# Kernel optimization log

Measured on AMD Instinct MI355X. Metric: run time of the kernel, lower is better.

## Reference

```python
import jax, jax.numpy as jnp
import numpy as np


def _swiglu(h):
    a, b = jnp.split(h, 2, axis=-1)
    return jax.nn.silu(a) * b


def setup_inputs() -> dict:
    key = jax.random.key(0)
    ks = jax.random.split(key, 12)
    B, T, D = 4, 2048, 1024
    HD = 4096          # dense FFN hidden (swiglu -> fc1 out 2*HD)
    S, K = 1024, 4     # ssm d_state, d_conv
    E, HE = 8, 512     # n_experts, expert hidden (swiglu)
    s = 0.02
    w = lambda k_, shape: jax.random.normal(k_, shape, jnp.float32) * s
    return dict(
        x=jax.random.normal(ks[0], (B, T, D), jnp.float32),
        rW=w(ks[1], (3, D)), rb=jnp.zeros((3,), jnp.float32),
        d1W=w(ks[2], (2 * HD, D)), d1b=jnp.zeros((2 * HD,), jnp.float32),
        d2W=w(ks[3], (D, HD)), d2b=jnp.zeros((D,), jnp.float32),
        sW_in=w(ks[4], (S, D)), sb_in=jnp.zeros((S,), jnp.float32),
        sW_conv=w(ks[5], (S, S, K)), sb_conv=jnp.zeros((S,), jnp.float32),
        sW_out=w(ks[6], (D, S)), sb_out=jnp.zeros((D,), jnp.float32),
        mW=w(ks[7], (E, D)), mb=jnp.zeros((E,), jnp.float32),
        eW1=w(ks[8], (E, 2 * HE, D)), eb1=jnp.zeros((E, 2 * HE), jnp.float32),
        eW2=w(ks[9], (E, D, HE)), eb2=jnp.zeros((E, D), jnp.float32),
        k=2,
    )


def reference(x, rW, rb, d1W, d1b, d2W, d2b,
              sW_in, sb_in, sW_conv, sb_conv, sW_out, sb_out,
              mW, mb, eW1, eb1, eW2, eb2, k):
    # ---- branch router (token-level softmax, temperature=1) ----
    bw = jax.nn.softmax(x @ rW.T + rb, axis=-1)              # [B,T,3]

    # ---- branch 0: dense swiglu FFN ----
    dense = _swiglu(x @ d1W.T + d1b) @ d2W.T + d2b           # [B,T,D]

    # ---- branch 1: SSM layer (causal conv, groups=1, gate=1) ----
    h = (x @ sW_in.T + sb_in).transpose(0, 2, 1)             # [B,S,T]
    Kc = sW_conv.shape[-1]
    conv = jax.lax.conv_general_dilated(
        h, sW_conv, window_strides=(1,), padding=[(Kc - 1, 0)],
        dimension_numbers=('NCH', 'OIH', 'NCH'))
    seq = (conv + sb_conv[None, :, None]).transpose(0, 2, 1)  # [B,T,S]
    ssm = seq @ sW_out.T + sb_out                             # [B,T,D]

    # ---- branch 2: MoE (top-k softmax router, dense-dispatch reference) ----
    E = mW.shape[0]
    logits = x @ mW.T + mb                                    # [B,T,E]
    vals, idx = jax.lax.top_k(logits, k)                      # [B,T,k]
    wk = jax.nn.softmax(vals, axis=-1)
    combine = jnp.sum(jax.nn.one_hot(idx, E, dtype=x.dtype) * wk[..., None], axis=-2)  # [B,T,E]
    h1 = _swiglu(jnp.einsum('btd,efd->btef', x, eW1) + eb1)   # [B,T,E,HE]
    eout = jnp.einsum('bteh,edh->bted', h1, eW2) + eb2        # [B,T,E,D]
    moe = jnp.einsum('bted,bte->btd', eout, combine)          # [B,T,D]

    return bw[..., 0:1] * dense + bw[..., 1:2] * ssm + bw[..., 2:3] * moe
```

## Files before the change

### kernel.cpp

```cpp
#include <hip/hip_runtime.h>
#include <hip/hip_bf16.h>
#include <cstdint>

typedef __bf16 bf16_t;
typedef __bf16 bf16x8 __attribute__((ext_vector_type(8)));
typedef float f32x4 __attribute__((ext_vector_type(4)));

#define DEV_INLINE __device__ __forceinline__

#define NTOK 8192
#define DDIM 1024
#define HDIM 4096
#define SDIM 1024
#define NEXP 8
#define HEXP 512
#define TSEQ 2048
#define MAXTILES 136
#define MAXROWS (MAXTILES * 128)

#define VMCNT(n) asm volatile("s_waitcnt vmcnt(" #n ")" ::: "memory")
#define BARF() asm volatile("s_barrier" ::: "memory")

__global__ __launch_bounds__(256) void k_f32_to_bf16(const float* __restrict__ src,
                                                     bf16_t* __restrict__ dst, int n8) {
  int i = blockIdx.x * 256 + threadIdx.x;
  if (i >= n8) return;
  const float4* s = (const float4*)src + (size_t)i * 2;
  float4 v0 = s[0], v1 = s[1];
  bf16x8 o;
  o[0] = (bf16_t)v0.x; o[1] = (bf16_t)v0.y; o[2] = (bf16_t)v0.z; o[3] = (bf16_t)v0.w;
  o[4] = (bf16_t)v1.x; o[5] = (bf16_t)v1.y; o[6] = (bf16_t)v1.z; o[7] = (bf16_t)v1.w;
  *((bf16x8*)dst + i) = o;
}

__global__ __launch_bounds__(256) void k_convw(const float* __restrict__ src,
                                               bf16_t* __restrict__ dst) {
  int i = blockIdx.x * 256 + threadIdx.x;
  size_t flat = (size_t)i * 8;
  int s = (int)(flat >> 12);
  int col = (int)(flat & 4095);
  int k = col >> 10;
  int si0 = col & 1023;
  const float* sp = src + (size_t)s * 4096 + k;
  bf16x8 o;
#pragma unroll
  for (int j = 0; j < 8; ++j) o[j] = (bf16_t)sp[(size_t)(si0 + j) * 4];
  *(bf16x8*)(dst + flat) = o;
}

__global__ __launch_bounds__(256) void k_im2col(const bf16_t* __restrict__ h,
                                                bf16_t* __restrict__ a2) {
  int i = blockIdx.x * 256 + threadIdx.x;
  size_t flat = (size_t)i * 8;
  int t = (int)(flat >> 12);
  int col = (int)(flat & 4095);
  int k = col >> 10;
  int si = col & 1023;
  int tt = t & (TSEQ - 1);
  bf16x8 v;
#pragma unroll
  for (int j = 0; j < 8; ++j) v[j] = (bf16_t)0.f;
  if (tt - 3 + k >= 0) v = *(const bf16x8*)(h + (size_t)(t - 3 + k) * SDIM + si);
  *(bf16x8*)(a2 + flat) = v;
}

__global__ __launch_bounds__(256) void k_zero(int* cnt, int* fill, int* idx,
                                              float* gate) {
  int i = blockIdx.x * 256 + threadIdx.x;
  if (i < NEXP) { cnt[i] = 0; fill[i] = 0; }
  if (i < MAXROWS) { idx[i] = 0; gate[i] = 0.f; }
}

__global__ __launch_bounds__(1024) void k_count(const int* __restrict__ top2e,
                                                int* __restrict__ cnt) {
  __shared__ int hist[NEXP];
  const int tid = threadIdx.x;
  if (tid < NEXP) hist[tid] = 0;
  __syncthreads();
  int c[NEXP];
#pragma unroll
  for (int e = 0; e < NEXP; ++e) c[e] = 0;
#pragma unroll
  for (int j = 0; j < 2 * NTOK / 1024; ++j) {
    int v = top2e[j * 1024 + tid];
#pragma unroll
    for (int e = 0; e < NEXP; ++e) c[e] += (v == e) ? 1 : 0;
  }
#pragma unroll
  for (int e = 0; e < NEXP; ++e)
    for (int off = 32; off; off >>= 1) c[e] += __shfl_xor(c[e], off);
  if ((tid & 63) == 0) {
#pragma unroll
    for (int e = 0; e < NEXP; ++e) atomicAdd(&hist[e], c[e]);
  }
  __syncthreads();
  if (tid < NEXP) cnt[tid] = hist[tid];
}

__global__ void k_scan(const int* __restrict__ cnt, int* __restrict__ base,
                       int* __restrict__ ntiles, int* __restrict__ tile_e,
                       int* __restrict__ tile_row) {
  if (threadIdx.x == 0 && blockIdx.x == 0) {
    int b = 0, tt = 0;
    for (int e = 0; e < NEXP; ++e) {
      base[e] = b;
      int nt = (cnt[e] + 127) >> 7;
      for (int j = 0; j < nt; ++j) { tile_e[tt] = e; tile_row[tt] = b + j * 128; ++tt; }
      b += nt * 128;
    }
    *ntiles = tt;
  }
}

__global__ __launch_bounds__(256) void k_scatter(const int* __restrict__ top2e,
                                                 const float* __restrict__ top2w,
                                                 const int* __restrict__ base,
                                                 int* __restrict__ fill,
                                                 int* __restrict__ idx,
                                                 float* __restrict__ gate) {
  __shared__ int lcnt[NEXP];
  __shared__ int lbase[NEXP];
  const int tid = threadIdx.x;
  const int t = blockIdx.x * 256 + tid;
  if (tid < NEXP) lcnt[tid] = 0;
  __syncthreads();
  const int e0 = top2e[t * 2 + 0], e1 = top2e[t * 2 + 1];
  const int s0 = atomicAdd(&lcnt[e0], 1);
  const int s1 = atomicAdd(&lcnt[e1], 1);
  __syncthreads();
  if (tid < NEXP) lbase[tid] = atomicAdd(&fill[tid], lcnt[tid]);
  __syncthreads();
  const int p0 = base[e0] + lbase[e0] + s0;
  const int p1 = base[e1] + lbase[e1] + s1;
  idx[p0] = t; gate[p0] = top2w[t * 2 + 0];
  idx[p1] = t; gate[p1] = top2w[t * 2 + 1];
}

__global__ __launch_bounds__(256) void k_router(const float* __restrict__ x,
                                                const float* __restrict__ rW,
                                                const float* __restrict__ rb,
                                                const float* __restrict__ mW,
                                                const float* __restrict__ mb,
                                                float* __restrict__ bw3,
                                                int* __restrict__ top2e,
                                                float* __restrict__ top2w) {
  int wave = threadIdx.x >> 6, lane = threadIdx.x & 63;
  int t = blockIdx.x * 4 + wave;
  const float* xr = x + (size_t)t * DDIM;
  float xv[16];
#pragma unroll
  for (int i = 0; i < 16; i += 4) *(float4*)&xv[i] = *(const float4*)&xr[lane * 16 + i];
  float acc[11];
#pragma unroll
  for (int j = 0; j < 11; ++j) {
    const float* w = (j < 3) ? (rW + j * DDIM) : (mW + (j - 3) * DDIM);
    float s = 0.f;
#pragma unroll
    for (int i = 0; i < 16; i += 4) {
      float4 wv = *(const float4*)&w[lane * 16 + i];
      s += xv[i] * wv.x + xv[i + 1] * wv.y + xv[i + 2] * wv.z + xv[i + 3] * wv.w;
    }
    acc[j] = s;
  }
#pragma unroll
  for (int j = 0; j < 11; ++j)
    for (int off = 32; off; off >>= 1) acc[j] += __shfl_xor(acc[j], off);
  if (lane == 0) {
    float l0 = acc[0] + rb[0], l1 = acc[1] + rb[1], l2 = acc[2] + rb[2];
    float mx = fmaxf(l0, fmaxf(l1, l2));
    float e0 = expf(l0 - mx), e1 = expf(l1 - mx), e2 = expf(l2 - mx);
    float inv = 1.f / (e0 + e1 + e2);
    float w2 = e2 * inv;
    bw3[t * 3 + 0] = e0 * inv; bw3[t * 3 + 1] = e1 * inv; bw3[t * 3 + 2] = w2;
    float lg[8];
#pragma unroll
    for (int e = 0; e < 8; ++e) lg[e] = acc[3 + e] + mb[e];
    int i0 = 0;
#pragma unroll
    for (int e = 1; e < 8; ++e) if (lg[e] > lg[i0]) i0 = e;
    int i1 = -1;
#pragma unroll
    for (int e = 0; e < 8; ++e) {
      if (e == i0) continue;
      if (i1 < 0 || lg[e] > lg[i1]) i1 = e;
    }
    float ee = expf(lg[i1] - lg[i0]);
    float w0 = 1.f / (1.f + ee), w1 = ee / (1.f + ee);
    top2e[t * 2 + 0] = i0; top2e[t * 2 + 1] = i1;
    top2w[t * 2 + 0] = w2 * w0; top2w[t * 2 + 1] = w2 * w1;
  }
}

DEV_INLINE void gload16(const bf16_t* g, bf16_t* l) {
  __builtin_amdgcn_global_load_lds((const __attribute__((address_space(1))) void*)g,
                                   (__attribute__((address_space(3))) void*)l, 16, 0, 0);
}

constexpr int EPI_BF16 = 0;
constexpr int EPI_OUT_W = 1;
constexpr int EPI_OUT_A = 2;
constexpr int EPI_SWIG = 4;
constexpr int EPI_SCAT = 5;

template <int EPI>
__global__ __launch_bounds__(256) void k_gemm(
    const bf16_t* __restrict__ A, const bf16_t* __restrict__ B,
    bf16_t* __restrict__ Cb, float* __restrict__ Cf,
    const float* __restrict__ bias, const float* __restrict__ scale, int sstride,
    const bf16_t* __restrict__ aux, int ldaux,
    int N, int K) {
  constexpr int BUF = 16384;
  __shared__ __align__(16) char lds[2 * BUF];

  const int tid = threadIdx.x;
  const int lane = tid & 63;
  const int wave = tid >> 6;
  const int lr = lane & 15;
  const int hi = lane >> 4;

  const int nbx = gridDim.x, nby = gridDim.y;
  int id = blockIdx.x + nbx * blockIdx.y;
  const int nwg = nbx * nby;
  if ((nwg & 7) == 0) id = (id & 7) * (nwg >> 3) + (id >> 3);
  const int bx = id % nbx;
  const int by = id / nbx;

  const int bm = by * 128;
  const int bn = bx * 128;
  const int wm = (wave >> 1) * 64;
  const int wn = (wave & 1) * 64;

  const int srow = tid >> 2;
  const int scol = 8 * ((tid & 3) ^ ((tid >> 3) & 3));
  const bf16_t* Asrc = A + (size_t)(bm + srow) * K + scol;
  const bf16_t* Bsrc = B + (size_t)(bn + srow) * K + scol;
  const size_t r64K = (size_t)64 * K;
  const int NT = K >> 5;

  f32x4 acc[4][4];
#pragma unroll
  for (int a = 0; a < 4; ++a)
#pragma unroll
    for (int b = 0; b < 4; ++b)
#pragma unroll
      for (int j = 0; j < 4; ++j) acc[a][b][j] = 0.f;

  auto stage = [&](int t) {
    char* l = lds + (t & 1) * BUF + tid * 16;
    const bf16_t* ga = Asrc + (size_t)t * 32;
    const bf16_t* gb = Bsrc + (size_t)t * 32;
    gload16(ga, (bf16_t*)l);
    gload16(ga + r64K, (bf16_t*)(l + 4096));
    gload16(gb, (bf16_t*)(l + 8192));
    gload16(gb + r64K, (bf16_t*)(l + 12288));
  };
  auto rdA = [&](int buf, int row) -> bf16x8 {
    int off = buf + (row << 6) + ((hi ^ ((row >> 1) & 3)) << 4);
    return *(const bf16x8*)(lds + off);
  };
  auto rdB = [&](int buf, int row) -> bf16x8 {
    int off = buf + 8192 + (row << 6) + ((hi ^ ((row >> 1) & 3)) << 4);
    return *(const bf16x8*)(lds + off);
  };

  stage(0);

  for (int t = 0; t < NT; ++t) {
    VMCNT(0);
    BARF();
    const int buf = (t & 1) * BUF;
    bf16x8 bfr[4], afr[4];
#pragma unroll
    for (int ni = 0; ni < 4; ++ni) bfr[ni] = rdB(buf, wn + ni * 16 + lr);
#pragma unroll
    for (int i = 0; i < 4; ++i) afr[i] = rdA(buf, wm + i * 16 + lr);
    if (t + 1 < NT) stage(t + 1);
    __builtin_amdgcn_s_setprio(1);
#pragma unroll
    for (int i = 0; i < 4; ++i)
#pragma unroll
      for (int ni = 0; ni < 4; ++ni)
        acc[i][ni] = __builtin_amdgcn_mfma_f32_16x16x32_bf16(afr[i], bfr[ni], acc[i][ni], 0, 0, 0);
    __builtin_amdgcn_s_setprio(0);
  }

  float bv[4];
#pragma unroll
  for (int ni = 0; ni < 4; ++ni) bv[ni] = bias[bn + wn + ni * 16 + lr];
#pragma unroll
  for (int mi = 0; mi < 4; ++mi) {
#pragma unroll
    for (int j = 0; j < 4; ++j) {
      const int rowg = bm + wm + mi * 16 + hi * 4 + j;
      float sc = 0.f;
      if constexpr (EPI == EPI_OUT_W || EPI == EPI_OUT_A)
        sc = scale[(size_t)rowg * sstride];
#pragma unroll
      for (int ni = 0; ni < 4; ++ni) {
        const int colg = bn + wn + ni * 16 + lr;
        float v = acc[mi][ni][j] + bv[ni];
        if constexpr (EPI == EPI_BF16) {
          Cb[(size_t)rowg * N + colg] = (bf16_t)v;
        } else if constexpr (EPI == EPI_OUT_W) {
          Cf[(size_t)rowg * N + colg] = sc * v;
        } else if constexpr (EPI == EPI_OUT_A) {
          Cf[(size_t)rowg * N + colg] += sc * v;
        } else {
          float bb = (float)aux[(size_t)rowg * ldaux + colg];
          float s = v / (1.f + __expf(-v));
          Cb[(size_t)rowg * N + colg] = (bf16_t)(s * bb);
        }
      }
    }
  }
}

template <int EPI, bool GA>
__global__ __launch_bounds__(256) void k_moe_gemm(
    const bf16_t* __restrict__ A, const bf16_t* __restrict__ Bw, size_t zB, int boff,
    bf16_t* __restrict__ Cb, float* __restrict__ Cf,
    const float* __restrict__ bias, int bstride,
    const bf16_t* __restrict__ aux,
    const int* __restrict__ ntiles_p, const int* __restrict__ tile_e,
    const int* __restrict__ tile_row, const int* __restrict__ idx,
    const float* __restrict__ gate,
    int N, int K) {
  constexpr int BUF = 16384;
  __shared__ __align__(16) char lds[2 * BUF];

  const int tid = threadIdx.x;
  const int lane = tid & 63;
  const int wave = tid >> 6;
  const int lr = lane & 15;
  const int hi = lane >> 4;

  const int nbx = gridDim.x, nby = gridDim.y;
  int id = blockIdx.x + nbx * blockIdx.y;
  const int nwg = nbx * nby;
  if ((nwg & 7) == 0) id = (id & 7) * (nwg >> 3) + (id >> 3);
  const int bx = id % nbx;
  const int by = id / nbx;

  const int ntiles = *ntiles_p;
  if (bx >= ntiles) return;
  const int e = tile_e[bx];
  const int bm = tile_row[bx];
  const int bn = by * 128;
  const int wm = (wave >> 1) * 64;
  const int wn = (wave & 1) * 64;

  const int srow = tid >> 2;
  const int scol = 8 * ((tid & 3) ^ ((tid >> 3) & 3));
  const int atok0 = GA ? idx[bm + srow] : (bm + srow);
  const int atok1 = GA ? idx[bm + srow + 64] : (bm + srow + 64);
  const bf16_t* Asrc0 = A + (size_t)atok0 * K + scol;
  const bf16_t* Asrc1 = A + (size_t)atok1 * K + scol;
  const bf16_t* Bsrc = Bw + (size_t)e * zB + (size_t)(boff + bn + srow) * K + scol;
  const size_t r64K = (size_t)64 * K;
  const int NT = K >> 5;

  f32x4 acc[4][4];
#pragma unroll
  for (int a = 0; a < 4; ++a)
#pragma unroll
    for (int b = 0; b < 4; ++b)
#pragma unroll
      for (int j = 0; j < 4; ++j) acc[a][b][j] = 0.f;

  auto stage = [&](int t) {
    char* l = lds + (t & 1) * BUF + tid * 16;
    gload16(Asrc0 + (size_t)t * 32, (bf16_t*)l);
    gload16(Asrc1 + (size_t)t * 32, (bf16_t*)(l + 4096));
    gload16(Bsrc + (size_t)t * 32, (bf16_t*)(l + 8192));
    gload16(Bsrc + (size_t)t * 32 + r64K, (bf16_t*)(l + 12288));
  };
  auto rdA = [&](int buf, int row) -> bf16x8 {
    int off = buf + (row << 6) + ((hi ^ ((row >> 1) & 3)) << 4);
    return *(const bf16x8*)(lds + off);
  };
  auto rdB = [&](int buf, int row) -> bf16x8 {
    int off = buf + 8192 + (row << 6) + ((hi ^ ((row >> 1) & 3)) << 4);
    return *(const bf16x8*)(lds + off);
  };

  stage(0);

  for (int t = 0; t < NT; ++t) {
    VMCNT(0);
    BARF();
    const int buf = (t & 1) * BUF;
    bf16x8 bfr[4], afr[4];
#pragma unroll
    for (int ni = 0; ni < 4; ++ni) bfr[ni] = rdB(buf, wn + ni * 16 + lr);
#pragma unroll
    for (int i = 0; i < 4; ++i) afr[i] = rdA(buf, wm + i * 16 + lr);
    if (t + 1 < NT) stage(t + 1);
    __builtin_amdgcn_s_setprio(1);
#pragma unroll
    for (int i = 0; i < 4; ++i)
#pragma unroll
      for (int ni = 0; ni < 4; ++ni)
        acc[i][ni] = __builtin_amdgcn_mfma_f32_16x16x32_bf16(afr[i], bfr[ni], acc[i][ni], 0, 0, 0);
    __builtin_amdgcn_s_setprio(0);
  }

  const float* bp = bias + (size_t)e * bstride + boff;
  float bv[4];
#pragma unroll
  for (int ni = 0; ni < 4; ++ni) bv[ni] = bp[bn + wn + ni * 16 + lr];
#pragma unroll
  for (int mi = 0; mi < 4; ++mi) {
#pragma unroll
    for (int j = 0; j < 4; ++j) {
      const int slot = bm + wm + mi * 16 + hi * 4 + j;
      float sc = 0.f;
      int tok = 0;
      if constexpr (EPI == EPI_SCAT) { sc = gate[slot]; tok = idx[slot]; }
#pragma unroll
      for (int ni = 0; ni < 4; ++ni) {
        const int colg = bn + wn + ni * 16 + lr;
        float v = acc[mi][ni][j] + bv[ni];
        if constexpr (EPI == EPI_BF16) {
          Cb[(size_t)slot * N + colg] = (bf16_t)v;
        } else if constexpr (EPI == EPI_SWIG) {
          float bb = (float)aux[(size_t)slot * N + colg];
          float s = v / (1.f + __expf(-v));
          Cb[(size_t)slot * N + colg] = (bf16_t)(s * bb);
        } else {
          if (sc != 0.f) atomicAdd(&Cf[(size_t)tok * N + colg], sc * v);
        }
      }
    }
  }
}

extern "C" void kernel_launch(void* const* d_in, const int* in_sizes, int n_in,
                              void* d_out, int out_size, void* d_ws, size_t ws_size,
                              hipStream_t stream) {
  (void)in_sizes; (void)n_in; (void)out_size; (void)ws_size;
  const float* x    = (const float*)d_in[0];
  const float* rW   = (const float*)d_in[1];
  const float* rb   = (const float*)d_in[2];
  const float* d1W  = (const float*)d_in[3];
  const float* d1b  = (const float*)d_in[4];
  const float* d2W  = (const float*)d_in[5];
  const float* d2b  = (const float*)d_in[6];
  const float* sWin = (const float*)d_in[7];
  const float* sbin = (const float*)d_in[8];
  const float* sWc  = (const float*)d_in[9];
  const float* sbc  = (const float*)d_in[10];
  const float* sWo  = (const float*)d_in[11];
  const float* sbo  = (const float*)d_in[12];
  const float* mW   = (const float*)d_in[13];
  const float* mb   = (const float*)d_in[14];
  const float* eW1  = (const float*)d_in[15];
  const float* eb1  = (const float*)d_in[16];
  const float* eW2  = (const float*)d_in[17];
  const float* eb2  = (const float*)d_in[18];
  float* out = (float*)d_out;

  char* ws = (char*)d_ws;
  size_t off = 0;
  auto alloc = [&](size_t bytes) -> void* {
    void* p = ws + off;
    off += (bytes + 255) & ~(size_t)255;
    return p;
  };
  bf16_t* xb    = (bf16_t*)alloc((size_t)NTOK * DDIM * 2);
  bf16_t* wd1   = (bf16_t*)alloc((size_t)2 * HDIM * DDIM * 2);
  bf16_t* wd2   = (bf16_t*)alloc((size_t)DDIM * HDIM * 2);
  bf16_t* wsin  = (bf16_t*)alloc((size_t)SDIM * DDIM * 2);
  bf16_t* wconv = (bf16_t*)alloc((size_t)SDIM * SDIM * 4 * 2);
  bf16_t* wsout = (bf16_t*)alloc((size_t)DDIM * SDIM * 2);
  bf16_t* we1   = (bf16_t*)alloc((size_t)NEXP * 2 * HEXP * DDIM * 2);
  bf16_t* we2   = (bf16_t*)alloc((size_t)NEXP * DDIM * HEXP * 2);
  bf16_t* Cc    = (bf16_t*)alloc((size_t)NTOK * HDIM * 2);
  bf16_t* Dd    = (bf16_t*)alloc((size_t)NTOK * HDIM * 2);
  bf16_t* th    = (bf16_t*)alloc((size_t)NTOK * SDIM * 2);
  bf16_t* tsq   = (bf16_t*)alloc((size_t)NTOK * SDIM * 2);
  float*  bw3   = (float*)alloc((size_t)NTOK * 3 * 4);
  int*    top2e = (int*)alloc((size_t)NTOK * 2 * 4);
  float*  top2w = (float*)alloc((size_t)NTOK * 2 * 4);
  int*    cnt   = (int*)alloc(NEXP * 4);
  int*    fill  = (int*)alloc(NEXP * 4);
  int*    basep = (int*)alloc((NEXP + 1) * 4);
  int*    ntl   = (int*)alloc(4);
  int*    t_e   = (int*)alloc(MAXTILES * 4);
  int*    t_row = (int*)alloc(MAXTILES * 4);
  int*    idx   = (int*)alloc(MAXROWS * 4);
  float*  gate  = (float*)alloc(MAXROWS * 4);

  k_f32_to_bf16<<<4096, 256, 0, stream>>>(x, xb, NTOK * DDIM / 8);
  k_f32_to_bf16<<<4096, 256, 0, stream>>>(d1W, wd1, 2 * HDIM * DDIM / 8);
  k_f32_to_bf16<<<2048, 256, 0, stream>>>(d2W, wd2, DDIM * HDIM / 8);
  k_f32_to_bf16<<<512, 256, 0, stream>>>(sWin, wsin, SDIM * DDIM / 8);
  k_convw<<<2048, 256, 0, stream>>>(sWc, wconv);
  k_f32_to_bf16<<<512, 256, 0, stream>>>(sWo, wsout, DDIM * SDIM / 8);
  k_f32_to_bf16<<<4096, 256, 0, stream>>>(eW1, we1, NEXP * 2 * HEXP * DDIM / 8);
  k_f32_to_bf16<<<2048, 256, 0, stream>>>(eW2, we2, NEXP * DDIM * HEXP / 8);
  k_zero<<<(MAXROWS + 255) / 256, 256, 0, stream>>>(cnt, fill, idx, gate);
  k_router<<<2048, 256, 0, stream>>>(x, rW, rb, mW, mb, bw3, top2e, top2w);
  k_count<<<1, 1024, 0, stream>>>(top2e, cnt);
  k_scan<<<1, 64, 0, stream>>>(cnt, basep, ntl, t_e, t_row);
  k_scatter<<<NTOK / 256, 256, 0, stream>>>(top2e, top2w, basep, fill, idx, gate);

  k_gemm<EPI_BF16><<<dim3(32, 64), 256, 0, stream>>>(
      xb, wd1 + (size_t)HDIM * DDIM, Dd, nullptr, d1b + HDIM, nullptr, 0, nullptr, 0,
      HDIM, DDIM);
  k_gemm<EPI_SWIG><<<dim3(32, 64), 256, 0, stream>>>(
      xb, wd1, Cc, nullptr, d1b, nullptr, 0, Dd, HDIM, HDIM, DDIM);
  k_gemm<EPI_OUT_W><<<dim3(8, 64), 256, 0, stream>>>(
      Cc, wd2, nullptr, out, d2b, bw3, 3, nullptr, 0, DDIM, HDIM);

  k_moe_gemm<EPI_BF16, true><<<dim3(MAXTILES, 4), 256, 0, stream>>>(
      xb, we1, (size_t)2 * HEXP * DDIM, HEXP, Dd, nullptr, eb1, 2 * HEXP, nullptr,
      ntl, t_e, t_row, idx, gate, HEXP, DDIM);
  k_moe_gemm<EPI_SWIG, true><<<dim3(MAXTILES, 4), 256, 0, stream>>>(
      xb, we1, (size_t)2 * HEXP * DDIM, 0, Cc, nullptr, eb1, 2 * HEXP, Dd,
      ntl, t_e, t_row, idx, gate, HEXP, DDIM);
  k_moe_gemm<EPI_SCAT, false><<<dim3(MAXTILES, 8), 256, 0, stream>>>(
      Cc, we2, (size_t)DDIM * HEXP, 0, nullptr, out, eb2, DDIM, nullptr,
      ntl, t_e, t_row, idx, gate, DDIM, HEXP);

  k_gemm<EPI_BF16><<<dim3(8, 64), 256, 0, stream>>>(
      xb, wsin, th, nullptr, sbin, nullptr, 0, nullptr, 0, SDIM, DDIM);
  k_im2col<<<16384, 256, 0, stream>>>(th, Dd);
  k_gemm<EPI_BF16><<<dim3(8, 64), 256, 0, stream>>>(
      Dd, wconv, tsq, nullptr, sbc, nullptr, 0, nullptr, 0, SDIM, SDIM * 4);
  k_gemm<EPI_OUT_A><<<dim3(8, 64), 256, 0, stream>>>(
      tsq, wsout, nullptr, out, sbo, bw3 + 1, 3, nullptr, 0, DDIM, SDIM);
}
```

Measured before the change: 680.7 us.

## Fuse im2col into conv GEMM, replace MoE atomic scatter with combine pass

Removes the im2col kernel by having a dedicated conv GEMM gather shifted rows of the SSM input directly into LDS, using a zero pad buffer for causal padding. The MoE down-projection now writes bf16 expert outputs per slot, and a separate combine kernel gathers each token's two slots and adds the gated sum into the output, replacing per-element float atomics. A supertile block remapping is also added for GEMMs with K up to 2048 to improve cache locality. This trades an extra bf16 intermediate write and read plus one more launch for removing atomic contention and the im2col buffer traffic.

After: 669.9 us. About the same (-1.6%).

```diff
diff --git a/kernel.cpp b/kernel.cpp
--- a/kernel.cpp
+++ b/kernel.cpp
@@ -48,27 +48,12 @@
   *(bf16x8*)(dst + flat) = o;
 }
 
-__global__ __launch_bounds__(256) void k_im2col(const bf16_t* __restrict__ h,
-                                                bf16_t* __restrict__ a2) {
-  int i = blockIdx.x * 256 + threadIdx.x;
-  size_t flat = (size_t)i * 8;
-  int t = (int)(flat >> 12);
-  int col = (int)(flat & 4095);
-  int k = col >> 10;
-  int si = col & 1023;
-  int tt = t & (TSEQ - 1);
-  bf16x8 v;
-#pragma unroll
-  for (int j = 0; j < 8; ++j) v[j] = (bf16_t)0.f;
-  if (tt - 3 + k >= 0) v = *(const bf16x8*)(h + (size_t)(t - 3 + k) * SDIM + si);
-  *(bf16x8*)(a2 + flat) = v;
-}
-
 __global__ __launch_bounds__(256) void k_zero(int* cnt, int* fill, int* idx,
-                                              float* gate) {
+                                              bf16_t* zpad) {
   int i = blockIdx.x * 256 + threadIdx.x;
   if (i < NEXP) { cnt[i] = 0; fill[i] = 0; }
-  if (i < MAXROWS) { idx[i] = 0; gate[i] = 0.f; }
+  if (i < 128) zpad[i] = (bf16_t)0.f;
+  if (i < MAXROWS) idx[i] = 0;
 }
 
 __global__ __launch_bounds__(1024) void k_count(const int* __restrict__ top2e,
@@ -117,7 +102,7 @@
                                                  const int* __restrict__ base,
                                                  int* __restrict__ fill,
                                                  int* __restrict__ idx,
-                                                 float* __restrict__ gate) {
+                                                 int* __restrict__ slotmap) {
   __shared__ int lcnt[NEXP];
   __shared__ int lbase[NEXP];
   const int tid = threadIdx.x;
@@ -132,8 +117,9 @@
   __syncthreads();
   const int p0 = base[e0] + lbase[e0] + s0;
   const int p1 = base[e1] + lbase[e1] + s1;
-  idx[p0] = t; gate[p0] = top2w[t * 2 + 0];
-  idx[p1] = t; gate[p1] = top2w[t * 2 + 1];
+  idx[p0] = t; idx[p1] = t;
+  slotmap[t * 2 + 0] = p0;
+  slotmap[t * 2 + 1] = p1;
 }
 
 __global__ __launch_bounds__(256) void k_router(const float* __restrict__ x,
@@ -191,16 +177,57 @@
   }
 }
 
+__global__ __launch_bounds__(256) void k_combine(const bf16_t* __restrict__ eo,
+                                                 const int* __restrict__ slotmap,
+                                                 const float* __restrict__ top2w,
+                                                 float* __restrict__ out) {
+  int wave = threadIdx.x >> 6, lane = threadIdx.x & 63;
+  int t = blockIdx.x * 4 + wave;
+  const int s0 = slotmap[t * 2 + 0], s1 = slotmap[t * 2 + 1];
+  const float g0 = top2w[t * 2 + 0], g1 = top2w[t * 2 + 1];
+  const bf16x8* r0 = (const bf16x8*)(eo + (size_t)s0 * DDIM);
+  const bf16x8* r1 = (const bf16x8*)(eo + (size_t)s1 * DDIM);
+  float* orow = out + (size_t)t * DDIM;
+#pragma unroll
+  for (int i = 0; i < 2; ++i) {
+    const int d = lane + i * 64;
+    bf16x8 a = r0[d], b = r1[d];
+    float vo[8];
+    *(float4*)&vo[0] = *(const float4*)&orow[d * 8];
+    *(float4*)&vo[4] = *(const float4*)&orow[d * 8 + 4];
+#pragma unroll
+    for (int j = 0; j < 8; ++j) vo[j] += g0 * (float)a[j] + g1 * (float)b[j];
+    *(float4*)&orow[d * 8] = *(float4*)&vo[0];
+    *(float4*)&orow[d * 8 + 4] = *(float4*)&vo[4];
+  }
+}
+
 DEV_INLINE void gload16(const bf16_t* g, bf16_t* l) {
   __builtin_amdgcn_global_load_lds((const __attribute__((address_space(1))) void*)g,
                                    (__attribute__((address_space(3))) void*)l, 16, 0, 0);
+}
+
+DEV_INLINE void blockmap(int K, int& bx, int& by) {
+  const int nbx = gridDim.x, nby = gridDim.y;
+  int id = blockIdx.x + nbx * blockIdx.y;
+  const int nwg = nbx * nby;
+  if ((nwg & 7) == 0) id = (id & 7) * (nwg >> 3) + (id >> 3);
+  if ((nbx & 3) == 0 && (nby & 7) == 0 && K <= 2048) {
+    const int nsx = nbx >> 2;
+    const int sx = id & 3, r = id >> 2;
+    const int sy = r & 7, st = r >> 3;
+    bx = (st % nsx) * 4 + sx;
+    by = (st / nsx) * 8 + sy;
+  } else {
+    bx = id % nbx;
+    by = id / nbx;
+  }
 }
 
 constexpr int EPI_BF16 = 0;
 constexpr int EPI_OUT_W = 1;
 constexpr int EPI_OUT_A = 2;
 constexpr int EPI_SWIG = 4;
-constexpr int EPI_SCAT = 5;
 
 template <int EPI>
 __global__ __launch_bounds__(256) void k_gemm(
@@ -218,12 +245,8 @@
   const int lr = lane & 15;
   const int hi = lane >> 4;
 
-  const int nbx = gridDim.x, nby = gridDim.y;
-  int id = blockIdx.x + nbx * blockIdx.y;
-  const int nwg = nbx * nby;
-  if ((nwg & 7) == 0) id = (id & 7) * (nwg >> 3) + (id >> 3);
-  const int bx = id % nbx;
-  const int by = id / nbx;
+  int bx, by;
+  blockmap(K, bx, by);
 
   const int bm = by * 128;
   const int bn = bx * 128;
@@ -315,15 +338,113 @@
   }
 }
 
+__global__ __launch_bounds__(256) void k_gemm_conv(
+    const bf16_t* __restrict__ h, const bf16_t* __restrict__ Bw,
+    bf16_t* __restrict__ Cb, const float* __restrict__ bias,
+    const bf16_t* __restrict__ zpad) {
+  constexpr int N = SDIM;
+  constexpr int K = SDIM * 4;
+  constexpr int BUF = 16384;
+  __shared__ __align__(16) char lds[2 * BUF];
+
+  const int tid = threadIdx.x;
+  const int lane = tid & 63;
+  const int wave = tid >> 6;
+  const int lr = lane & 15;
+  const int hi = lane >> 4;
+
+  int bx, by;
+  blockmap(K, bx, by);
+
+  const int bm = by * 128;
+  const int bn = bx * 128;
+  const int wm = (wave >> 1) * 64;
+  const int wn = (wave & 1) * 64;
+
+  const int srow = tid >> 2;
+  const int scol = 8 * ((tid & 3) ^ ((tid >> 3) & 3));
+  const int row0 = bm + srow;
+  const int tt0 = row0 & (TSEQ - 1);
+  const bf16_t* Bsrc = Bw + (size_t)(bn + srow) * K + scol;
+  const size_t r64K = (size_t)64 * K;
+  const int NT = K >> 5;
+
+  f32x4 acc[4][4];
+#pragma unroll
+  for (int a = 0; a < 4; ++a)
+#pragma unroll
+    for (int b = 0; b < 4; ++b)
+#pragma unroll
+      for (int j = 0; j < 4; ++j) acc[a][b][j] = 0.f;
+
+  auto stage = [&](int t) {
+    char* l = lds + (t & 1) * BUF + tid * 16;
+    const int k = t >> 5;
+    const int si = (t & 31) * 32 + scol;
+    const bf16_t* ga0 = (tt0 + k >= 3)
+        ? h + (size_t)(row0 + k - 3) * SDIM + si : zpad;
+    const bf16_t* ga1 = h + (size_t)(row0 + 64 + k - 3) * SDIM + si;
+    gload16(ga0, (bf16_t*)l);
+    gload16(ga1, (bf16_t*)(l + 4096));
+    const bf16_t* gb = Bsrc + (size_t)t * 32;
+    gload16(gb, (bf16_t*)(l + 8192));
+    gload16(gb + r64K, (bf16_t*)(l + 12288));
+  };
+  auto rdA = [&](int buf, int row) -> bf16x8 {
+    int off = buf + (row << 6) + ((hi ^ ((row >> 1) & 3)) << 4);
+    return *(const bf16x8*)(lds + off);
+  };
+  auto rdB = [&](int buf, int row) -> bf16x8 {
+    int off = buf + 8192 + (row << 6) + ((hi ^ ((row >> 1) & 3)) << 4);
+    return *(const bf16x8*)(lds + off);
+  };
+
+  stage(0);
+
+  for (int t = 0; t < NT; ++t) {
+    VMCNT(0);
+    BARF();
+    const int buf = (t & 1) * BUF;
+    bf16x8 bfr[4], afr[4];
+#pragma unroll
+    for (int ni = 0; ni < 4; ++ni) bfr[ni] = rdB(buf, wn + ni * 16 + lr);
+#pragma unroll
+    for (int i = 0; i < 4; ++i) afr[i] = rdA(buf, wm + i * 16 + lr);
+    if (t + 1 < NT) stage(t + 1);
+    __builtin_amdgcn_s_setprio(1);
+#pragma unroll
+    for (int i = 0; i < 4; ++i)
+#pragma unroll
+      for (int ni = 0; ni < 4; ++ni)
+        acc[i][ni] = __builtin_amdgcn_mfma_f32_16x16x32_bf16(afr[i], bfr[ni], acc[i][ni], 0, 0, 0);
+    __builtin_amdgcn_s_setprio(0);
+  }
+
+  float bv[4];
+#pragma unroll
+  for (int ni = 0; ni < 4; ++ni) bv[ni] = bias[bn + wn + ni * 16 + lr];
+#pragma unroll
+  for (int mi = 0; mi < 4; ++mi) {
+#pragma unroll
+    for (int j = 0; j < 4; ++j) {
+      const int rowg = bm + wm + mi * 16 + hi * 4 + j;
+#pragma unroll
+      for (int ni = 0; ni < 4; ++ni) {
+        const int colg = bn + wn + ni * 16 + lr;
+        Cb[(size_t)rowg * N + colg] = (bf16_t)(acc[mi][ni][j] + bv[ni]);
+      }
+    }
+  }
+}
+
 template <int EPI, bool GA>
 __global__ __launch_bounds__(256) void k_moe_gemm(
     const bf16_t* __restrict__ A, const bf16_t* __restrict__ Bw, size_t zB, int boff,
-    bf16_t* __restrict__ Cb, float* __restrict__ Cf,
+    bf16_t* __restrict__ Cb,
     const float* __restrict__ bias, int bstride,
     const bf16_t* __restrict__ aux,
     const int* __restrict__ ntiles_p, const int* __restrict__ tile_e,
     const int* __restrict__ tile_row, const int* __restrict__ idx,
-    const float* __restrict__ gate,
     int N, int K) {
   constexpr int BUF = 16384;
   __shared__ __align__(16) char lds[2 * BUF];
@@ -413,21 +534,16 @@
 #pragma unroll
     for (int j = 0; j < 4; ++j) {
       const int slot = bm + wm + mi * 16 + hi * 4 + j;
-      float sc = 0.f;
-      int tok = 0;
-      if constexpr (EPI == EPI_SCAT) { sc = gate[slot]; tok = idx[slot]; }
 #pragma unroll
       for (int ni = 0; ni < 4; ++ni) {
         const int colg = bn + wn + ni * 16 + lr;
         float v = acc[mi][ni][j] + bv[ni];
         if constexpr (EPI == EPI_BF16) {
           Cb[(size_t)slot * N + colg] = (bf16_t)v;
-        } else if constexpr (EPI == EPI_SWIG) {
+        } else {
           float bb = (float)aux[(size_t)slot * N + colg];
           float s = v / (1.f + __expf(-v));
           Cb[(size_t)slot * N + colg] = (bf16_t)(s * bb);
-        } else {
-          if (sc != 0.f) atomicAdd(&Cf[(size_t)tok * N + colg], sc * v);
         }
       }
     }
@@ -481,6 +597,7 @@
   float*  bw3   = (float*)alloc((size_t)NTOK * 3 * 4);
   int*    top2e = (int*)alloc((size_t)NTOK * 2 * 4);
   float*  top2w = (float*)alloc((size_t)NTOK * 2 * 4);
+  int*    slotm = (int*)alloc((size_t)NTOK * 2 * 4);
   int*    cnt   = (int*)alloc(NEXP * 4);
   int*    fill  = (int*)alloc(NEXP * 4);
   int*    basep = (int*)alloc((NEXP + 1) * 4);
@@ -488,7 +605,8 @@
   int*    t_e   = (int*)alloc(MAXTILES * 4);
   int*    t_row = (int*)alloc(MAXTILES * 4);
   int*    idx   = (int*)alloc(MAXROWS * 4);
-  float*  gate  = (float*)alloc(MAXROWS * 4);
+  bf16_t* zpad  = (bf16_t*)alloc(256);
+  bf16_t* eo    = Dd;
 
   k_f32_to_bf16<<<4096, 256, 0, stream>>>(x, xb, NTOK * DDIM / 8);
   k_f32_to_bf16<<<4096, 256, 0, stream>>>(d1W, wd1, 2 * HDIM * DDIM / 8);
@@ -498,11 +616,11 @@
   k_f32_to_bf16<<<512, 256, 0, stream>>>(sWo, wsout, DDIM * SDIM / 8);
   k_f32_to_bf16<<<4096, 256, 0, stream>>>(eW1, we1, NEXP * 2 * HEXP * DDIM / 8);
   k_f32_to_bf16<<<2048, 256, 0, stream>>>(eW2, we2, NEXP * DDIM * HEXP / 8);
-  k_zero<<<(MAXROWS + 255) / 256, 256, 0, stream>>>(cnt, fill, idx, gate);
+  k_zero<<<(MAXROWS + 255) / 256, 256, 0, stream>>>(cnt, fill, idx, zpad);
   k_router<<<2048, 256, 0, stream>>>(x, rW, rb, mW, mb, bw3, top2e, top2w);
   k_count<<<1, 1024, 0, stream>>>(top2e, cnt);
   k_scan<<<1, 64, 0, stream>>>(cnt, basep, ntl, t_e, t_row);
-  k_scatter<<<NTOK / 256, 256, 0, stream>>>(top2e, top2w, basep, fill, idx, gate);
+  k_scatter<<<NTOK / 256, 256, 0, stream>>>(top2e, top2w, basep, fill, idx, slotm);
 
   k_gemm<EPI_BF16><<<dim3(32, 64), 256, 0, stream>>>(
       xb, wd1 + (size_t)HDIM * DDIM, Dd, nullptr, d1b + HDIM, nullptr, 0, nullptr, 0,
@@ -513,20 +631,19 @@
       Cc, wd2, nullptr, out, d2b, bw3, 3, nullptr, 0, DDIM, HDIM);
 
   k_moe_gemm<EPI_BF16, true><<<dim3(MAXTILES, 4), 256, 0, stream>>>(
-      xb, we1, (size_t)2 * HEXP * DDIM, HEXP, Dd, nullptr, eb1, 2 * HEXP, nullptr,
-      ntl, t_e, t_row, idx, gate, HEXP, DDIM);
+      xb, we1, (size_t)2 * HEXP * DDIM, HEXP, Dd, eb1, 2 * HEXP, nullptr,
+      ntl, t_e, t_row, idx, HEXP, DDIM);
   k_moe_gemm<EPI_SWIG, true><<<dim3(MAXTILES, 4), 256, 0, stream>>>(
-      xb, we1, (size_t)2 * HEXP * DDIM, 0, Cc, nullptr, eb1, 2 * HEXP, Dd,
-      ntl, t_e, t_row, idx, gate, HEXP, DDIM);
-  k_moe_gemm<EPI_SCAT, false><<<dim3(MAXTILES, 8), 256, 0, stream>>>(
-      Cc, we2, (size_t)DDIM * HEXP, 0, nullptr, out, eb2, DDIM, nullptr,
-      ntl, t_e, t_row, idx, gate, DDIM, HEXP);
+      xb, we1, (size_t)2 * HEXP * DDIM, 0, Cc, eb1, 2 * HEXP, Dd,
+      ntl, t_e, t_row, idx, HEXP, DDIM);
+  k_moe_gemm<EPI_BF16, false><<<dim3(MAXTILES, 8), 256, 0, stream>>>(
+      Cc, we2, (size_t)DDIM * HEXP, 0, eo, eb2, DDIM, nullptr,
+      ntl, t_e, t_row, idx, DDIM, HEXP);
+  k_combine<<<NTOK / 4, 256, 0, stream>>>(eo, slotm, top2w, out);
 
   k_gemm<EPI_BF16><<<dim3(8, 64), 256, 0, stream>>>(
       xb, wsin, th, nullptr, sbin, nullptr, 0, nullptr, 0, SDIM, DDIM);
-  k_im2col<<<16384, 256, 0, stream>>>(th, Dd);
-  k_gemm<EPI_BF16><<<dim3(8, 64), 256, 0, stream>>>(
-      Dd, wconv, tsq, nullptr, sbc, nullptr, 0, nullptr, 0, SDIM, SDIM * 4);
+  k_gemm_conv<<<dim3(8, 64), 256, 0, stream>>>(th, wconv, tsq, sbc, zpad);
   k_gemm<EPI_OUT_A><<<dim3(8, 64), 256, 0, stream>>>(
       tsq, wsout, nullptr, out, sbo, bw3 + 1, 3, nullptr, 0, DDIM, SDIM);
 }
```
